# Optimization experiments

Hardware: AMD Instinct MI355X
Metric: run time of the kernel (lower is better)

## Reference

```python
import jax, jax.numpy as jnp
import numpy as np

RADIUS = 0.1
K_NEIGHBOURS = 32


def setup_inputs() -> dict:
    key = jax.random.key(0)
    k1, k2, k3 = jax.random.split(key, 3)
    B, N, M, C = 4, 8192, 2048, 128
    xyz = jax.random.uniform(k1, (B, 3, N), dtype=jnp.float32)
    new_xyz = jax.random.uniform(k2, (B, 3, M), dtype=jnp.float32)
    feature = jax.random.normal(k3, (B, C, N), dtype=jnp.float32)
    return {"new_xyz": new_xyz, "xyz": xyz, "feature": feature, "use_xyz": 1}


def _ball_query(xyz, new_xyz, radius, k):
    # xyz: [B,3,N], new_xyz: [B,3,M] -> idx [B,M,k] (first-k-in-ball, padded
    # with first valid index, pointnet2 semantics), counts [B,M]
    n = xyz.shape[-1]
    # squared pairwise distance [B,M,N]
    d2 = jnp.sum((new_xyz[:, :, :, None] - xyz[:, :, None, :]) ** 2, axis=1)
    in_ball = d2 < radius * radius
    cand = jnp.where(in_ball, jnp.arange(n, dtype=jnp.int32), n)
    # smallest indices first == first-k points inside the ball
    idx_sorted = jnp.sort(cand, axis=-1)[..., :k]
    valid = idx_sorted < n
    first = idx_sorted[..., :1]
    pad = jnp.where(first < n, first, 0)  # empty ball -> index 0
    idx = jnp.where(valid, idx_sorted, pad).astype(jnp.int32)
    count = jnp.sum(valid, axis=-1).astype(jnp.int32)
    return idx, count


def _group_points(f, idx):
    # f: [B,C,N], idx: [B,M,K] -> [B,C,M,K]
    return jax.vmap(lambda fb, ib: fb[:, ib])(f, idx)


def reference(new_xyz, xyz, feature, use_xyz):
    idx, _count = _ball_query(xyz, new_xyz, RADIUS, K_NEIGHBOURS)
    group_xyz = _group_points(xyz, idx) - new_xyz[..., None]  # [B,3,M,K]
    group_feature = _group_points(feature, idx)               # [B,C,M,K]
    if use_xyz:
        group_feature = jnp.concatenate([group_xyz, group_feature], axis=1)
    return group_feature, group_xyz
```

## Files before the change

kernel.cpp:

```cpp
#include <hip/hip_runtime.h>
#include <hip/hip_bf16.h>


#define K_NEIGH 32
#define R2_F32 0.009999999776482582f
#define CCH 128
#define NPTS 8192
#define MQ 2048

__global__ __launch_bounds__(256, 8) void ball_split4_kernel(
    const float* __restrict__ xyz,
    const float* __restrict__ new_xyz,
    int* __restrict__ idxb,
    float* __restrict__ out0,
    float* __restrict__ out1,
    int use_xyz)
{
    __shared__ int scnt[4][4];
    __shared__ int sff [4][4];
    __shared__ int slidx[4][4][K_NEIGH];

    const int tid  = threadIdx.x;
    const int w    = tid >> 6;
    const int lane = tid & 63;
    const int q0 = blockIdx.x * 4;
    const int b  = q0 / MQ;
    const int m0 = q0 - b * MQ;

    const float* x0 = xyz + (size_t)b * 3 * NPTS;
    const float* x1 = x0 + NPTS;
    const float* x2 = x1 + NPTS;
    const float* nb = new_xyz + (size_t)b * 3 * MQ;

    float qx[4], qy[4], qz[4];
    #pragma unroll
    for (int j = 0; j < 4; ++j) {
        qx[j] = nb[m0 + j];
        qy[j] = nb[MQ + m0 + j];
        qz[j] = nb[2 * MQ + m0 + j];
    }
    int cnt[4] = {0, 0, 0, 0};
    int ff [4] = {0, 0, 0, 0};
    const unsigned long long below = (1ull << lane) - 1ull;

    const int rbase = w * 2048;
    for (int g = 0; g < 2048; g += 64) {
        const int i = rbase + g + lane;
        const float ax = x0[i];
        const float ay = x1[i];
        const float az = x2[i];
        #pragma unroll
        for (int j = 0; j < 4; ++j) {
            const float d2 = __fadd_rn(__fadd_rn(__fmul_rn(ax - qx[j], ax - qx[j]),
                                                 __fmul_rn(ay - qy[j], ay - qy[j])),
                                       __fmul_rn(az - qz[j], az - qz[j]));
            const bool in = d2 < R2_F32;
            const unsigned long long mk = __ballot(in);
            if (mk) {
                if (cnt[j] == 0) ff[j] = rbase + g + (__ffsll(mk) - 1);
                if (in) {
                    const int pos = cnt[j] + __popcll(mk & below);
                    if (pos < K_NEIGH) slidx[w][j][pos] = i;
                }
                cnt[j] += __popcll(mk);
            }
        }
    }

    if (lane < 4) {
        scnt[w][lane] = cnt[lane];
        sff [w][lane] = ff[lane];
    }
    __syncthreads();

    const int jq = w;
    const float qxx = nb[m0 + jq];
    const float qyy = nb[MQ + m0 + jq];
    const float qzz = nb[2 * MQ + m0 + jq];

    if (lane < K_NEIGH) {
        int bacc = 0, jdx = -1, ffq = 0;
        bool ffset = false;
        #pragma unroll
        for (int r = 0; r < 4; ++r) {
            const int cr = scnt[r][jq];
            if (!ffset && cr > 0) { ffq = sff[r][jq]; ffset = true; }
            if (jdx < 0 && lane < bacc + cr) jdx = slidx[r][jq][lane - bacc];
            bacc += cr;
        }
        if (jdx < 0) jdx = ffq;

        const int m = m0 + jq;
        idxb[((size_t)b * MQ + m) * K_NEIGH + lane] = jdx;
        const float gx = x0[jdx] - qxx;
        const float gy = x1[jdx] - qyy;
        const float gz = x2[jdx] - qzz;
        const size_t MK = (size_t)MQ * K_NEIGH;
        const size_t o1 = (size_t)b * 3 * MK + (size_t)m * K_NEIGH + lane;
        out1[o1]          = gx;
        out1[o1 + MK]     = gy;
        out1[o1 + 2 * MK] = gz;
        if (use_xyz) {
            const size_t o0 = (size_t)b * (CCH + 3) * MK + (size_t)m * K_NEIGH + lane;
            out0[o0]          = gx;
            out0[o0 + MK]     = gy;
            out0[o0 + 2 * MK] = gz;
        }
    }
}

__global__ __launch_bounds__(256) void ball_query_xyz_kernel(
    const float* __restrict__ xyz, const float* __restrict__ new_xyz,
    int* __restrict__ idxb, float* __restrict__ out0, float* __restrict__ out1,
    int N, int M, int C, int use_xyz)
{
    __shared__ int lidx[4][K_NEIGH];
    const int wave = threadIdx.x >> 6;
    const int lane = threadIdx.x & 63;
    const int q = blockIdx.x * 4 + wave;
    const int b = q / M;
    const int m = q - b * M;

    const float* xb = xyz + (size_t)b * 3 * N;
    const float* x0 = xb;
    const float* x1 = xb + N;
    const float* x2 = xb + 2 * N;
    const float* nb = new_xyz + (size_t)b * 3 * M;
    const float qx = nb[m];
    const float qy = nb[M + m];
    const float qz = nb[2 * M + m];

    int cnt = 0;
    int ff  = 0;
    const unsigned long long below = (1ull << lane) - 1ull;

    for (int t0 = 0; t0 < N; t0 += 64) {
        const int i = t0 + lane;
        const float dx = x0[i] - qx;
        const float dy = x1[i] - qy;
        const float dz = x2[i] - qz;
        const float d2 = __fadd_rn(__fadd_rn(__fmul_rn(dx, dx), __fmul_rn(dy, dy)),
                                   __fmul_rn(dz, dz));
        const bool in_ball = d2 < R2_F32;
        const unsigned long long mask = __ballot(in_ball);
        if (mask) {
            if (cnt == 0) ff = t0 + (__ffsll(mask) - 1);
            if (in_ball) {
                const int pos = cnt + __popcll(mask & below);
                if (pos < K_NEIGH) lidx[wave][pos] = i;
            }
            cnt += __popcll(mask);
            if (cnt >= K_NEIGH) break;
        }
    }

    asm volatile("s_waitcnt lgkmcnt(0)" ::: "memory");

    if (lane < K_NEIGH) {
        const int j = (lane < cnt) ? lidx[wave][lane] : ff;
        idxb[(size_t)q * K_NEIGH + lane] = j;
        const float gx = x0[j] - qx;
        const float gy = x1[j] - qy;
        const float gz = x2[j] - qz;
        const size_t MK = (size_t)M * K_NEIGH;
        const size_t o1 = (size_t)b * 3 * MK + (size_t)m * K_NEIGH + lane;
        out1[o1]          = gx;
        out1[o1 + MK]     = gy;
        out1[o1 + 2 * MK] = gz;
        if (use_xyz) {
            const size_t o0 = (size_t)b * (C + 3) * MK + (size_t)m * K_NEIGH + lane;
            out0[o0]          = gx;
            out0[o0 + MK]     = gy;
            out0[o0 + 2 * MK] = gz;
        }
    }
}

__global__ __launch_bounds__(1024, 4) void gather_onepass_kernel(
    const float* __restrict__ feat,
    const int* __restrict__ idxb,
    float* __restrict__ out0,
    int use_xyz)
{
    __shared__ float sf[2 * NPTS];

    const int t   = threadIdx.x;
    const int bid = blockIdx.x;
    const int b   = (bid & 7) >> 1;
    const int cg  = ((bid >> 3) << 1) | (bid & 1);
    const int c0  = cg * 2;

    const int4* ip4 = (const int4*)(idxb + (size_t)b * MQ * K_NEIGH);
    int4 jj[16];
    #pragma unroll
    for (int i = 0; i < 16; ++i) jj[i] = ip4[i * 1024 + t];

    const float4* fv = (const float4*)(feat + ((size_t)b * CCH + c0) * NPTS);
    #pragma unroll
    for (int r = 0; r < 4; ++r)
        ((float4*)sf)[t + r * 1024] = fv[t + r * 1024];
    __syncthreads();

    const size_t MK = (size_t)MQ * K_NEIGH;
    const int CO   = use_xyz ? (CCH + 3) : CCH;
    const int coff = use_xyz ? 3 : 0;
    float* o0 = out0 + ((size_t)b * CO + coff + c0) * MK;
    float* o1 = o0 + MK;

    #pragma unroll
    for (int i = 0; i < 16; ++i) {
        const int p = i * 4096 + 4 * t;
        const int4 j4 = jj[i];
        float4 s0, s1;
        s0.x = sf[j4.x]; s0.y = sf[j4.y]; s0.z = sf[j4.z]; s0.w = sf[j4.w];
        s1.x = sf[NPTS + j4.x]; s1.y = sf[NPTS + j4.y];
        s1.z = sf[NPTS + j4.z]; s1.w = sf[NPTS + j4.w];
        *(float4*)(o0 + p) = s0;
        *(float4*)(o1 + p) = s1;
    }
}

__global__ __launch_bounds__(256) void gather_kernel(
    const float* __restrict__ xyz, const float* __restrict__ new_xyz,
    const float* __restrict__ feat, const int* __restrict__ idxb,
    float* __restrict__ out0, float* __restrict__ out1,
    int N, int M, int C, int use_xyz)
{
    const int tid = threadIdx.x;
    const int k = tid & 31;
    const int mloc = tid >> 5;
    const int mchunks = M >> 3;
    const int b = blockIdx.x / mchunks;
    const int m = (blockIdx.x - b * mchunks) * 8 + mloc;
    const int q = b * M + m;
    const int j = idxb[(size_t)q * K_NEIGH + k];
    const size_t xb = (size_t)b * 3 * N;
    const size_t nb = (size_t)b * 3 * M;
    const float gx = xyz[xb + j]         - new_xyz[nb + m];
    const float gy = xyz[xb + N + j]     - new_xyz[nb + M + m];
    const float gz = xyz[xb + 2 * N + j] - new_xyz[nb + 2 * M + m];
    const size_t MK = (size_t)M * K_NEIGH;
    const size_t o1 = (size_t)b * 3 * MK + (size_t)m * K_NEIGH + k;
    out1[o1] = gx; out1[o1 + MK] = gy; out1[o1 + 2 * MK] = gz;
    const int CO = use_xyz ? (C + 3) : C;
    size_t o0 = (size_t)b * CO * MK + (size_t)m * K_NEIGH + k;
    if (use_xyz) {
        out0[o0] = gx; out0[o0 + MK] = gy; out0[o0 + 2 * MK] = gz;
        o0 += 3 * MK;
    }
    const float* fb = feat + (size_t)b * C * N;
    #pragma unroll 4
    for (int c = 0; c < C; c += 4) {
        const float v0 = fb[(size_t)c * N + j];
        const float v1 = fb[(size_t)(c + 1) * N + j];
        const float v2 = fb[(size_t)(c + 2) * N + j];
        const float v3 = fb[(size_t)(c + 3) * N + j];
        out0[o0 + (size_t)c * MK]       = v0;
        out0[o0 + (size_t)(c + 1) * MK] = v1;
        out0[o0 + (size_t)(c + 2) * MK] = v2;
        out0[o0 + (size_t)(c + 3) * MK] = v3;
    }
}

extern "C" void kernel_launch(void* const* d_in, const int* in_sizes, int n_in,
                              void* d_out, int out_size, void* d_ws, size_t ws_size,
                              hipStream_t stream) {
    const float* new_xyz = (const float*)d_in[0];
    const float* xyz     = (const float*)d_in[1];
    const float* feat    = (const float*)d_in[2];

    const int B = 4;
    const int M = in_sizes[0] / (3 * B);
    const int N = in_sizes[1] / (3 * B);
    const int C = in_sizes[2] / (B * N);

    const long long sz_with = (long long)B * (C + 6) * M * K_NEIGH;
    const int use_xyz = (out_size == sz_with) ? 1 : 0;

    float* out0 = (float*)d_out;
    float* out1 = out0 + (size_t)B * (use_xyz ? (C + 3) : C) * M * K_NEIGH;

    int* idxb = (int*)d_ws;
    const size_t idx_bytes = (size_t)B * M * K_NEIGH * sizeof(int);

    const bool fast = (B == 4) && (N == NPTS) && (M == MQ) && (C == CCH)
                      && (ws_size >= idx_bytes);

    if (fast) {
        ball_split4_kernel<<<(B * MQ) / 4, 256, 0, stream>>>(
            xyz, new_xyz, idxb, out0, out1, use_xyz);
        gather_onepass_kernel<<<256, 1024, 0, stream>>>(feat, idxb, out0, use_xyz);
    } else {
        ball_query_xyz_kernel<<<(B * M) / 4, 256, 0, stream>>>(
            xyz, new_xyz, idxb, out0, out1, N, M, C, use_xyz);
        gather_kernel<<<B * (M / 8), 256, 0, stream>>>(xyz, new_xyz, feat, idxb,
                                                       out0, out1, N, M, C, use_xyz);
    }
}
```

Measured before the change: 53.46 us.

## Restructure ball query to one query per lane with partitioned scan and merge

```diff
diff --git a/kernel.cpp b/kernel.cpp
--- a/kernel.cpp
+++ b/kernel.cpp
@@ -8,104 +8,122 @@
 #define NPTS 8192
 #define MQ 2048
 
-__global__ __launch_bounds__(256, 8) void ball_split4_kernel(
+__global__ __launch_bounds__(1024, 8) void ball_scan_kernel(
     const float* __restrict__ xyz,
     const float* __restrict__ new_xyz,
-    int* __restrict__ idxb,
-    float* __restrict__ out0,
-    float* __restrict__ out1,
-    int use_xyz)
-{
-    __shared__ int scnt[4][4];
-    __shared__ int sff [4][4];
-    __shared__ int slidx[4][4][K_NEIGH];
+    int* __restrict__ part)
+{
+    __shared__ int s_slot[16][64][16];
+    __shared__ int s_cnt[16][64];
 
     const int tid  = threadIdx.x;
-    const int w    = tid >> 6;
+    const int wv   = __builtin_amdgcn_readfirstlane(tid >> 6);
     const int lane = tid & 63;
-    const int q0 = blockIdx.x * 4;
-    const int b  = q0 / MQ;
-    const int m0 = q0 - b * MQ;
+    const int qg   = blockIdx.x >> 2;
+    const int pr   = blockIdx.x & 3;
+    const int b    = qg >> 5;
+    const int m    = ((qg & 31) << 6) + lane;
 
     const float* x0 = xyz + (size_t)b * 3 * NPTS;
     const float* x1 = x0 + NPTS;
     const float* x2 = x1 + NPTS;
     const float* nb = new_xyz + (size_t)b * 3 * MQ;
-
-    float qx[4], qy[4], qz[4];
-    #pragma unroll
-    for (int j = 0; j < 4; ++j) {
-        qx[j] = nb[m0 + j];
-        qy[j] = nb[MQ + m0 + j];
-        qz[j] = nb[2 * MQ + m0 + j];
-    }
-    int cnt[4] = {0, 0, 0, 0};
-    int ff [4] = {0, 0, 0, 0};
-    const unsigned long long below = (1ull << lane) - 1ull;
-
-    const int rbase = w * 2048;
-    for (int g = 0; g < 2048; g += 64) {
-        const int i = rbase + g + lane;
+    const float qx = nb[m];
+    const float qy = nb[MQ + m];
+    const float qz = nb[2 * MQ + m];
+
+    int cnt = 0;
+    const int ibase = pr * 2048 + wv * 128;
+    #pragma unroll 8
+    for (int p = 0; p < 128; ++p) {
+        const int i = ibase + p;
         const float ax = x0[i];
         const float ay = x1[i];
         const float az = x2[i];
-        #pragma unroll
-        for (int j = 0; j < 4; ++j) {
-            const float d2 = __fadd_rn(__fadd_rn(__fmul_rn(ax - qx[j], ax - qx[j]),
-                                                 __fmul_rn(ay - qy[j], ay - qy[j])),
-                                       __fmul_rn(az - qz[j], az - qz[j]));
-            const bool in = d2 < R2_F32;
-            const unsigned long long mk = __ballot(in);
-            if (mk) {
-                if (cnt[j] == 0) ff[j] = rbase + g + (__ffsll(mk) - 1);
-                if (in) {
-                    const int pos = cnt[j] + __popcll(mk & below);
-                    if (pos < K_NEIGH) slidx[w][j][pos] = i;
-                }
-                cnt[j] += __popcll(mk);
+        const float dx = ax - qx;
+        const float dy = ay - qy;
+        const float dz = az - qz;
+        const float d2 = __fadd_rn(__fadd_rn(__fmul_rn(dx, dx), __fmul_rn(dy, dy)),
+                                   __fmul_rn(dz, dz));
+        if (d2 < R2_F32) {
+            if (cnt < 16) s_slot[wv][lane][cnt] = i;
+            ++cnt;
+        }
+    }
+    s_cnt[wv][lane] = (cnt < 16) ? cnt : 16;
+    __syncthreads();
+
+    const int q_local = tid >> 4;
+    const int k2 = tid & 15;
+
+    int total = 0;
+    #pragma unroll
+    for (int w = 0; w < 16; ++w) total += s_cnt[w][q_local];
+    const int qcnt = (total < K_NEIGH) ? total : K_NEIGH;
+
+    const int q = (qg << 6) + q_local;
+    int* pq = part + ((size_t)q * 4 + pr) * 33;
+    if (k2 == 0) pq[0] = qcnt;
+
+    #pragma unroll
+    for (int half = 0; half < 2; ++half) {
+        const int s = k2 + half * 16;
+        if (s < qcnt) {
+            int accw = 0, pw = 0, po = 0, found = 0;
+            #pragma unroll
+            for (int w = 0; w < 16; ++w) {
+                const int cw = s_cnt[w][q_local];
+                if (!found && s < accw + cw) { pw = w; po = s - accw; found = 1; }
+                accw += cw;
             }
+            pq[1 + s] = s_slot[pw][q_local][po];
         }
     }
-
-    if (lane < 4) {
-        scnt[w][lane] = cnt[lane];
-        sff [w][lane] = ff[lane];
-    }
-    __syncthreads();
-
-    const int jq = w;
-    const float qxx = nb[m0 + jq];
-    const float qyy = nb[MQ + m0 + jq];
-    const float qzz = nb[2 * MQ + m0 + jq];
-
-    if (lane < K_NEIGH) {
-        int bacc = 0, jdx = -1, ffq = 0;
-        bool ffset = false;
-        #pragma unroll
-        for (int r = 0; r < 4; ++r) {
-            const int cr = scnt[r][jq];
-            if (!ffset && cr > 0) { ffq = sff[r][jq]; ffset = true; }
-            if (jdx < 0 && lane < bacc + cr) jdx = slidx[r][jq][lane - bacc];
-            bacc += cr;
-        }
-        if (jdx < 0) jdx = ffq;
-
-        const int m = m0 + jq;
-        idxb[((size_t)b * MQ + m) * K_NEIGH + lane] = jdx;
-        const float gx = x0[jdx] - qxx;
-        const float gy = x1[jdx] - qyy;
-        const float gz = x2[jdx] - qzz;
-        const size_t MK = (size_t)MQ * K_NEIGH;
-        const size_t o1 = (size_t)b * 3 * MK + (size_t)m * K_NEIGH + lane;
-        out1[o1]          = gx;
-        out1[o1 + MK]     = gy;
-        out1[o1 + 2 * MK] = gz;
-        if (use_xyz) {
-            const size_t o0 = (size_t)b * (CCH + 3) * MK + (size_t)m * K_NEIGH + lane;
-            out0[o0]          = gx;
-            out0[o0 + MK]     = gy;
-            out0[o0 + 2 * MK] = gz;
-        }
+}
+
+__global__ __launch_bounds__(256) void ball_final_kernel(
+    const float* __restrict__ xyz, const float* __restrict__ new_xyz,
+    const int* __restrict__ part, int* __restrict__ idxb,
+    float* __restrict__ out0, float* __restrict__ out1, int use_xyz)
+{
+    const int t = blockIdx.x * 256 + threadIdx.x;
+    const int q = t >> 5;
+    const int s = t & 31;
+    const int b = q >> 11;
+    const int m = q & (MQ - 1);
+
+    const int* P = part + (size_t)q * 4 * 33;
+    const int c0 = P[0], c1 = P[33], c2 = P[66], c3 = P[99];
+    const int total = c0 + c1 + c2 + c3;
+
+    int j = 0;
+    if (total > 0) {
+        const int ss = (s < total) ? s : 0;
+        int pr, off;
+        if (ss < c0)                { pr = 0; off = ss; }
+        else if (ss < c0 + c1)      { pr = 1; off = ss - c0; }
+        else if (ss < c0 + c1 + c2) { pr = 2; off = ss - c0 - c1; }
+        else                        { pr = 3; off = ss - c0 - c1 - c2; }
+        j = P[pr * 33 + 1 + off];
+    }
+
+    idxb[(size_t)q * K_NEIGH + s] = j;
+
+    const float* x0 = xyz + (size_t)b * 3 * NPTS;
+    const float* nb = new_xyz + (size_t)b * 3 * MQ;
+    const float gx = x0[j]            - nb[m];
+    const float gy = x0[NPTS + j]     - nb[MQ + m];
+    const float gz = x0[2 * NPTS + j] - nb[2 * MQ + m];
+    const size_t MK = (size_t)MQ * K_NEIGH;
+    const size_t o1 = (size_t)b * 3 * MK + (size_t)m * K_NEIGH + s;
+    out1[o1]          = gx;
+    out1[o1 + MK]     = gy;
+    out1[o1 + 2 * MK] = gz;
+    if (use_xyz) {
+        const size_t o0 = (size_t)b * (CCH + 3) * MK + (size_t)m * K_NEIGH + s;
+        out0[o0]          = gx;
+        out0[o0 + MK]     = gy;
+        out0[o0 + 2 * MK] = gz;
     }
 }
 
@@ -281,14 +299,17 @@
     float* out1 = out0 + (size_t)B * (use_xyz ? (C + 3) : C) * M * K_NEIGH;
 
     int* idxb = (int*)d_ws;
-    const size_t idx_bytes = (size_t)B * M * K_NEIGH * sizeof(int);
+    const size_t idx_bytes  = (size_t)B * M * K_NEIGH * sizeof(int);
+    int* part = (int*)((char*)d_ws + idx_bytes);
+    const size_t part_bytes = (size_t)B * M * 4 * 33 * sizeof(int);
 
     const bool fast = (B == 4) && (N == NPTS) && (M == MQ) && (C == CCH)
-                      && (ws_size >= idx_bytes);
+                      && (ws_size >= idx_bytes + part_bytes);
 
     if (fast) {
-        ball_split4_kernel<<<(B * MQ) / 4, 256, 0, stream>>>(
-            xyz, new_xyz, idxb, out0, out1, use_xyz);
+        ball_scan_kernel<<<512, 1024, 0, stream>>>(xyz, new_xyz, part);
+        ball_final_kernel<<<(B * MQ * K_NEIGH) / 256, 256, 0, stream>>>(
+            xyz, new_xyz, part, idxb, out0, out1, use_xyz);
         gather_onepass_kernel<<<256, 1024, 0, stream>>>(feat, idxb, out0, use_xyz);
     } else {
         ball_query_xyz_kernel<<<(B * M) / 4, 256, 0, stream>>>(
```

Measured after the change: 72.05 us. +34.8%, slower.
